# Kernel optimization log

Hardware: AMD Instinct MI355X
Metric: run time of the kernel (lower is better)

The kernel has to match this reference:

```python
import jax, jax.numpy as jnp
import numpy as np

TEMP = 0.1          # temp1 == base_temperature -> scale factor temp/base = 1
N_VIEW = 100        # max_views


def _select_indices(hard, easy):
    """Deterministic analogue of _hard_anchor_sampling's per-(image,class) pick.
    hard, easy: [M, HW] bool. Returns [M, N_VIEW] pixel indices (hard first,
    then easy, in pixel-index order; torch uses randperm but the contrastive
    loss is invariant to which/ordering of in-set samples)."""
    half = N_VIEW // 2
    nh = hard.sum(-1)
    ne = easy.sum(-1)
    both = (nh >= half) & (ne >= half)
    hk = jnp.where(both, half, jnp.where(nh >= half, N_VIEW - ne, nh))  # num_hard_keep
    ek = N_VIEW - hk                                                     # num_easy_keep
    hrank = jnp.cumsum(hard.astype(jnp.int32), -1) - 1
    erank = jnp.cumsum(easy.astype(jnp.int32), -1) - 1
    sel = (hard & (hrank < hk[:, None])) | (easy & (erank < ek[:, None]))
    # stable argsort puts selected pixels first, preserving index order
    order = jnp.argsort(jnp.where(sel, 0, 1), axis=-1)
    return order[:, :N_VIEW]


def _contrastive(feats_, labels_):
    """feats_: [A, V, D], labels_: [A] float. Supervised contrastive loss."""
    A, V, D = feats_.shape
    N = A * V
    # torch.cat(torch.unbind(feats_, 1), 0) -> view-major ordering
    cf = feats_.transpose(1, 0, 2).reshape(N, D)
    lab = jnp.tile(labels_, V)                           # mask.repeat(V, V)
    mask = (lab[:, None] == lab[None, :]).astype(cf.dtype)
    logits = (cf @ cf.T) / TEMP                          # [N, N]
    logits = logits - jax.lax.stop_gradient(logits.max(axis=1, keepdims=True))
    neg_mask = 1.0 - mask                                # before removing diagonal
    pos_mask = mask * (1.0 - jnp.eye(N, dtype=cf.dtype)) # logits_mask zeroes diag
    exp_l = jnp.exp(logits)
    neg_sum = (exp_l * neg_mask).sum(axis=1, keepdims=True)
    log_prob = logits - jnp.log(exp_l + neg_sum)
    mean_log_prob_pos = (pos_mask * log_prob).sum(axis=1) / pos_mask.sum(axis=1)
    return -(TEMP / TEMP) * mean_log_prob_pos.mean()


def _forward(feats, predict, labels):
    B, D, H, W = feats.shape
    C = predict.shape[1]
    HW = H * W
    # F.normalize(feats, p=2, dim=1)
    norm = jnp.sqrt((feats * feats).sum(axis=1, keepdims=True))
    feats = feats / jnp.maximum(norm, 1e-12)
    # bilinear upsample of logits to (H, W), softmax, conf/argmax
    logits_up = jax.image.resize(predict, (B, C, H, W), method='linear')
    probs = jax.nn.softmax(logits_up, axis=1)
    pred = jnp.argmax(probs, axis=1)                     # [B, H, W] (conf unused by loss)
    # nearest resize of labels to (H, W) is identity here (same size)
    pred_f = pred.reshape(B, HW)
    lab_f = labels.reshape(B, HW)
    feats_f = feats.transpose(0, 2, 3, 1).reshape(B, HW, D)
    cls = jnp.arange(C)
    hard = (pred_f[:, None, :] == cls[None, :, None]) & (lab_f[:, None, :] != cls[None, :, None])
    easy = (pred_f[:, None, :] == cls[None, :, None]) & (lab_f[:, None, :] == cls[None, :, None])
    idx = _select_indices(hard.reshape(B * C, HW), easy.reshape(B * C, HW))  # [B*C, N_VIEW]
    b_idx = jnp.repeat(jnp.arange(B), C)
    X_ = feats_f[b_idx[:, None], idx]                    # [B*C, N_VIEW, D]
    y_ = jnp.tile(cls, B).astype(feats.dtype)            # [B*C]
    return _contrastive(X_, y_)


def setup_inputs() -> dict:
    key = jax.random.key(0)
    k1, k2, k3 = jax.random.split(key, 3)
    feats = jax.random.normal(k1, (4, 256, 128, 128), dtype=jnp.float32)
    predict = jax.random.normal(k2, (4, 21, 64, 64), dtype=jnp.float32)
    labels = jax.random.randint(k3, (4, 128, 128), 0, 21, dtype=jnp.int32)
    return {"feats": feats, "predict": predict, "labels": labels}


def reference(feats, predict, labels):
    return _forward(feats, predict, labels)
```

## Files before the change

### kernel.cpp

```cpp
#include <hip/hip_runtime.h>
#include <math.h>

#define HW 16384
#define WID 128
#define BB 4
#define CC 21
#define DD 256
#define NA 84
#define NV 100
#define NN 8400
#define NPOS 400
#define NPAD 8448
#define NTILE 66

typedef __bf16 bf16;
typedef bf16 v8bf __attribute__((ext_vector_type(8)));
typedef float v4f __attribute__((ext_vector_type(4)));

#define AS1(p) ((const __attribute__((address_space(1))) void*)(p))
#define AS3(p) ((__attribute__((address_space(3))) void*)(p))

__global__ void pred_kernel(const float* __restrict__ predict, int* __restrict__ pred) {
  int t = blockIdx.x * blockDim.x + threadIdx.x;
  int b = t / HW;
  int p = t % HW;
  int y = p / WID, x = p % WID;
  float yin = y * 0.5f - 0.25f;
  float xin = x * 0.5f - 0.25f;
  int y0 = (int)floorf(yin), x0 = (int)floorf(xin);
  float fy = yin - (float)y0, fx = xin - (float)x0;
  int y0c = max(y0, 0), y1c = min(y0 + 1, 63);
  int x0c = max(x0, 0), x1c = min(x0 + 1, 63);
  float w00 = (1.f - fy) * (1.f - fx), w01 = (1.f - fy) * fx;
  float w10 = fy * (1.f - fx),        w11 = fy * fx;
  const float* pb = predict + (size_t)b * CC * 4096;
  float best = -1e30f; int bc = 0;
  for (int c = 0; c < CC; ++c) {
    const float* pc = pb + c * 4096;
    float v = w00 * pc[y0c * 64 + x0c] + w01 * pc[y0c * 64 + x1c]
            + w10 * pc[y1c * 64 + x0c] + w11 * pc[y1c * 64 + x1c];
    if (v > best) { best = v; bc = c; }
  }
  pred[t] = bc;
}

__global__ __launch_bounds__(256) void select_kernel(const int* __restrict__ pred,
                                                     const int* __restrict__ labels,
                                                     int* __restrict__ idx) {
  int pair = blockIdx.x;
  int b = pair / CC, c = pair % CC;
  int tid = threadIdx.x;
  const int4* pb = (const int4*)(pred + b * HW) + tid * 16;
  const int4* lb = (const int4*)(labels + b * HW) + tid * 16;

  unsigned long long hm = 0ull, em = 0ull;
  #pragma unroll
  for (int g = 0; g < 16; ++g) {
    int4 p4 = pb[g];
    int4 l4 = lb[g];
    unsigned long long h =
        ((unsigned long long)((p4.x == c) & (l4.x != c)))      |
        ((unsigned long long)((p4.y == c) & (l4.y != c)) << 1) |
        ((unsigned long long)((p4.z == c) & (l4.z != c)) << 2) |
        ((unsigned long long)((p4.w == c) & (l4.w != c)) << 3);
    unsigned long long e =
        ((unsigned long long)((p4.x == c) & (l4.x == c)))      |
        ((unsigned long long)((p4.y == c) & (l4.y == c)) << 1) |
        ((unsigned long long)((p4.z == c) & (l4.z == c)) << 2) |
        ((unsigned long long)((p4.w == c) & (l4.w == c)) << 3);
    hm |= h << (g * 4);
    em |= e << (g * 4);
  }
  int nh_t = __popcll(hm), ne_t = __popcll(em);

  __shared__ int sh[256], se[256], ss[256];
  sh[tid] = nh_t; se[tid] = ne_t;
  __syncthreads();
  for (int off = 1; off < 256; off <<= 1) {
    int vh = (tid >= off) ? sh[tid - off] : 0;
    int ve = (tid >= off) ? se[tid - off] : 0;
    __syncthreads();
    sh[tid] += vh; se[tid] += ve;
    __syncthreads();
  }
  int h_excl = sh[tid] - nh_t, e_excl = se[tid] - ne_t;
  int nh = sh[255], ne = se[255];

  const int half = NV / 2;
  int hk;
  if (nh >= half && ne >= half) hk = half;
  else if (nh >= half)          hk = NV - ne;
  else                          hk = nh;
  int ek = NV - hk;

  int takeh = min(max(hk - h_excl, 0), nh_t);
  int takee = min(max(ek - e_excl, 0), ne_t);
  int sel_t = takeh + takee;
  ss[tid] = sel_t;
  __syncthreads();
  for (int off = 1; off < 256; off <<= 1) {
    int vs = (tid >= off) ? ss[tid - off] : 0;
    __syncthreads();
    ss[tid] += vs;
    __syncthreads();
  }
  int s_excl = ss[tid] - sel_t;
  int total_sel = ss[255];
  int F = NV - total_sel;
  int u_excl = tid * 64 - s_excl;

  int* out = idx + pair * NV;
  int sc = 0, uc = 0, hc = 0, ec = 0;
  for (int l = 0; l < 64; ++l) {
    int p = tid * 64 + l;
    int hard = (int)((hm >> l) & 1ull);
    int easy = (int)((em >> l) & 1ull);
    bool sel = (hard && hc < takeh) || (easy && ec < takee);
    hc += hard; ec += easy;
    if (sel) {
      if (s_excl + sc < NV) out[s_excl + sc] = p;
      sc++;
    } else {
      if (u_excl + uc < F) out[total_sel + u_excl + uc] = p;
      uc++;
    }
  }
}

__global__ __launch_bounds__(256) void gather_kernel(const float* __restrict__ feats,
                                                     const int* __restrict__ idx,
                                                     bf16* __restrict__ cf) {
  int g = blockIdx.x;
  int a = g % NA;
  int v0 = (g / NA) * 4;
  int b = a / CC;
  int d = threadIdx.x;

  int p[4];
  #pragma unroll
  for (int k = 0; k < 4; ++k) p[k] = idx[a * NV + v0 + k];
  const float* base = feats + (size_t)(b * DD + d) * HW;
  float val[4], ssk[4];
  #pragma unroll
  for (int k = 0; k < 4; ++k) { val[k] = base[p[k]]; ssk[k] = val[k] * val[k]; }

  #pragma unroll
  for (int k = 0; k < 4; ++k) {
    float s = ssk[k];
    s += __shfl_xor(s, 1);  s += __shfl_xor(s, 2);  s += __shfl_xor(s, 4);
    s += __shfl_xor(s, 8);  s += __shfl_xor(s, 16); s += __shfl_xor(s, 32);
    ssk[k] = s;
  }
  __shared__ float red[4][4];
  if ((d & 63) == 0) {
    #pragma unroll
    for (int k = 0; k < 4; ++k) red[d >> 6][k] = ssk[k];
  }
  __syncthreads();
  #pragma unroll
  for (int k = 0; k < 4; ++k) {
    float tot = red[0][k] + red[1][k] + red[2][k] + red[3][k];
    float inv = 1.0f / fmaxf(sqrtf(tot), 1e-12f);
    int n = (v0 + k) * NA + a;
    cf[(size_t)n * DD + d] = (bf16)(val[k] * inv);
  }
}

__global__ __launch_bounds__(256) void gemm_kernel(const bf16* __restrict__ cf,
                                                   float* __restrict__ row_part) {
  __shared__ __align__(16) bf16 smem[2 * 128 * 64];
  bf16* sA = smem;
  bf16* sB = smem + 128 * 64;
  int i0 = blockIdx.y * 128;
  int j0 = blockIdx.x * 128;
  int tid = threadIdx.x;
  int wave = tid >> 6, lane = tid & 63;
  int wi = wave >> 1, wj = wave & 1;
  int m = lane & 15, q = lane >> 4;

  v4f acc[4][4] = {};

  int lrow = lane >> 3;
  int lcol = (lane & 7) * 8;

  for (int k0 = 0; k0 < DD; k0 += 64) {
    #pragma unroll
    for (int it = 0; it < 4; ++it) {
      int row = wave * 32 + it * 8;
      const bf16* gA = cf + (size_t)(i0 + row + lrow) * DD + k0 + lcol;
      const bf16* gB = cf + (size_t)(j0 + row + lrow) * DD + k0 + lcol;
      __builtin_amdgcn_global_load_lds(AS1(gA), AS3(sA + row * 64), 16, 0, 0);
      __builtin_amdgcn_global_load_lds(AS1(gB), AS3(sB + row * 64), 16, 0, 0);
    }
    __syncthreads();
    #pragma unroll
    for (int kk = 0; kk < 2; ++kk) {
      v8bf af[4], bfr[4];
      #pragma unroll
      for (int tt = 0; tt < 4; ++tt)
        af[tt] = *(const v8bf*)(sA + (wi * 64 + tt * 16 + m) * 64 + kk * 32 + q * 8);
      #pragma unroll
      for (int tt = 0; tt < 4; ++tt)
        bfr[tt] = *(const v8bf*)(sB + (wj * 64 + tt * 16 + m) * 64 + kk * 32 + q * 8);
      #pragma unroll
      for (int ti = 0; ti < 4; ++ti)
        #pragma unroll
        for (int tj = 0; tj < 4; ++tj)
          acc[ti][tj] = __builtin_amdgcn_mfma_f32_16x16x32_bf16(af[ti], bfr[tj], acc[ti][tj], 0, 0, 0);
    }
    __syncthreads();
  }

  int jw0 = j0 + wj * 64;

  float rowp[16];
  #pragma unroll
  for (int tt = 0; tt < 16; ++tt) rowp[tt] = 0.f;

  #pragma unroll
  for (int ti = 0; ti < 4; ++ti) {
    #pragma unroll
    for (int r = 0; r < 4; ++r) {
      #pragma unroll
      for (int tj = 0; tj < 4; ++tj) {
        int j = jw0 + tj * 16 + m;
        if (j >= NN) continue;
        rowp[ti * 4 + r] += __expf(acc[ti][tj][r] * 10.0f - 10.0f);
      }
    }
  }

  float* red = (float*)smem;
  #pragma unroll
  for (int ti = 0; ti < 4; ++ti)
    #pragma unroll
    for (int r = 0; r < 4; ++r) {
      int rg = wi * 64 + ti * 16 + q * 4 + r;
      red[rg * 33 + wj * 16 + m] = rowp[ti * 4 + r];
    }
  __syncthreads();
  if (tid < 128) {
    float s = 0.f;
    #pragma unroll
    for (int t = 0; t < 32; ++t) s += red[tid * 33 + t];
    row_part[(size_t)blockIdx.x * NPAD + i0 + tid] = s;
  }
}

__global__ __launch_bounds__(256) void pos_gemm_kernel(const bf16* __restrict__ cf,
                                                       float* __restrict__ s_pos) {
  __shared__ __align__(16) bf16 smem[2 * 128 * 64];
  bf16* sA = smem;
  bf16* sB = smem + 128 * 64;
  int c = blockIdx.y;
  int bx = blockIdx.x;
  int i0r = (bx >> 2) * 128;
  int j0r = (bx & 3) * 128;
  int tid = threadIdx.x;
  int wave = tid >> 6, lane = tid & 63;
  int wi = wave >> 1, wj = wave & 1;
  int m = lane & 15, q = lane >> 4;

  v4f acc[4][4] = {};

  int lrow = lane >> 3;
  int lcol = (lane & 7) * 8;

  for (int k0 = 0; k0 < DD; k0 += 64) {
    #pragma unroll
    for (int it = 0; it < 4; ++it) {
      int row = wave * 32 + it * 8;
      int ri = i0r + row + lrow, rj = j0r + row + lrow;
      int gi = (ri < NPOS) ? ((ri >> 2) * NA + (ri & 3) * CC + c) : NN;
      int gj = (rj < NPOS) ? ((rj >> 2) * NA + (rj & 3) * CC + c) : NN;
      const bf16* gA = cf + (size_t)gi * DD + k0 + lcol;
      const bf16* gB = cf + (size_t)gj * DD + k0 + lcol;
      __builtin_amdgcn_global_load_lds(AS1(gA), AS3(sA + row * 64), 16, 0, 0);
      __builtin_amdgcn_global_load_lds(AS1(gB), AS3(sB + row * 64), 16, 0, 0);
    }
    __syncthreads();
    #pragma unroll
    for (int kk = 0; kk < 2; ++kk) {
      v8bf af[4], bfr[4];
      #pragma unroll
      for (int tt = 0; tt < 4; ++tt)
        af[tt] = *(const v8bf*)(sA + (wi * 64 + tt * 16 + m) * 64 + kk * 32 + q * 8);
      #pragma unroll
      for (int tt = 0; tt < 4; ++tt)
        bfr[tt] = *(const v8bf*)(sB + (wj * 64 + tt * 16 + m) * 64 + kk * 32 + q * 8);
      #pragma unroll
      for (int ti = 0; ti < 4; ++ti)
        #pragma unroll
        for (int tj = 0; tj < 4; ++tj)
          acc[ti][tj] = __builtin_amdgcn_mfma_f32_16x16x32_bf16(af[ti], bfr[tj], acc[ti][tj], 0, 0, 0);
    }
    __syncthreads();
  }

  #pragma unroll
  for (int ti = 0; ti < 4; ++ti) {
    #pragma unroll
    for (int r = 0; r < 4; ++r) {
      int ri = i0r + wi * 64 + ti * 16 + q * 4 + r;
      if (ri >= NPOS) continue;
      int gi = (ri >> 2) * NA + (ri & 3) * CC + c;
      #pragma unroll
      for (int tj = 0; tj < 4; ++tj) {
        int rj = j0r + wj * 64 + tj * 16 + m;
        if (rj < NPOS)
          s_pos[(size_t)gi * NPOS + rj] = acc[ti][tj][r] * 10.0f - 10.0f;
      }
    }
  }
}

__global__ __launch_bounds__(256) void loss_kernel(const float* __restrict__ s_pos,
                                                   const float* __restrict__ row_part,
                                                   double* __restrict__ partials) {
  int tid = threadIdx.x;
  int wave = tid >> 6, lane = tid & 63;
  int i = blockIdx.x * 4 + wave;
  const float* row = s_pos + (size_t)i * NPOS;

  float nsum = 0.f;
  for (int jb = lane; jb < NTILE; jb += 64)
    nsum += row_part[(size_t)jb * NPAD + i];

  float sp[7], ev[7];
  float psum = 0.f;
  #pragma unroll
  for (int t = 0; t < 7; ++t) {
    int k = lane + t * 64;
    if (k < NPOS) {
      sp[t] = row[k];
      ev[t] = __expf(sp[t]);
      psum += ev[t];
    } else { sp[t] = 0.f; ev[t] = 0.f; }
  }
  float comb = nsum - psum;
  for (int o = 32; o; o >>= 1) comb += __shfl_xor(comb, o);
  float ns = comb;

  int self = (i / NA) * 4 + ((i % NA) / CC);
  float tsum = 0.f;
  #pragma unroll
  for (int t = 0; t < 7; ++t) {
    int k = lane + t * 64;
    if (k < NPOS && k != self)
      tsum += sp[t] - __logf(ev[t] + ns);
  }
  for (int o = 32; o; o >>= 1) tsum += __shfl_xor(tsum, o);

  __shared__ float r2[4];
  if (lane == 0) r2[wave] = tsum;
  __syncthreads();
  if (tid == 0) partials[blockIdx.x] = (double)(r2[0] + r2[1] + r2[2] + r2[3]);
}

__global__ void final_kernel(const double* __restrict__ partials, float* __restrict__ out) {
  int lane = threadIdx.x;
  double s = 0.0;
  for (int t = lane; t < 2100; t += 64) s += partials[t];
  for (int o = 32; o; o >>= 1) s += __shfl_down(s, o);
  if (lane == 0) out[0] = (float)(-s / 399.0 / 8400.0);
}

extern "C" void kernel_launch(void* const* d_in, const int* in_sizes, int n_in,
                              void* d_out, int out_size, void* d_ws, size_t ws_size,
                              hipStream_t stream) {
  const float* feats   = (const float*)d_in[0];
  const float* predict = (const float*)d_in[1];
  const int*   labels  = (const int*)d_in[2];
  float* out = (float*)d_out;
  char* ws = (char*)d_ws;

  int*    pred     = (int*)(ws + 0);
  int*    idx      = (int*)(ws + 262144);
  float*  row_part = (float*)(ws + 295744);
  double* partials = (double*)(ws + 2526016);
  bf16*   cf       = (bf16*)(ws + 2542816);
  float*  s_pos    = (float*)(ws + 6868192);

  (void)hipMemsetAsync((char*)(cf + (size_t)NN * DD), 0, (size_t)(NPAD - NN) * DD * 2, stream);

  pred_kernel<<<256, 256, 0, stream>>>(predict, pred);
  select_kernel<<<NA, 256, 0, stream>>>(pred, labels, idx);
  gather_kernel<<<2100, 256, 0, stream>>>(feats, idx, cf);
  gemm_kernel<<<dim3(NTILE, NTILE), 256, 0, stream>>>(cf, row_part);
  pos_gemm_kernel<<<dim3(16, CC), 256, 0, stream>>>(cf, s_pos);
  loss_kernel<<<2100, 256, 0, stream>>>(s_pos, row_part, partials);
  final_kernel<<<1, 64, 0, stream>>>(partials, out);
}
```

Measured before the change: 209.7 us.

## Merge positive-pair GEMM into main GEMM launch and XOR-swizzle LDS tiles

Folds the per-class positive-pair GEMM blocks into the main Gram-matrix kernel as extra blocks in a 1D grid, which removes one kernel launch and lets the small pos tiles fill idle CUs in the tail. It also applies an XOR swizzle to the 16-byte column chunks during global->LDS loads and the matching fragment reads, to cut LDS bank conflicts on the MFMA operand loads. The cost is a branch on block type and some extra index arithmetic.

```diff
diff --git a/kernel.cpp b/kernel.cpp
--- a/kernel.cpp
+++ b/kernel.cpp
@@ -12,6 +12,8 @@
 #define NPOS 400
 #define NPAD 8448
 #define NTILE 66
+#define NSQ (NTILE * NTILE)
+#define NPOSBLK (16 * CC)
 
 typedef __bf16 bf16;
 typedef bf16 v8bf __attribute__((ext_vector_type(8)));
@@ -167,12 +169,24 @@
 }
 
 __global__ __launch_bounds__(256) void gemm_kernel(const bf16* __restrict__ cf,
-                                                   float* __restrict__ row_part) {
+                                                   float* __restrict__ row_part,
+                                                   float* __restrict__ s_pos) {
   __shared__ __align__(16) bf16 smem[2 * 128 * 64];
   bf16* sA = smem;
   bf16* sB = smem + 128 * 64;
-  int i0 = blockIdx.y * 128;
-  int j0 = blockIdx.x * 128;
+  int blk = blockIdx.x;
+  bool pos = blk >= NSQ;
+  int i0, j0, c = 0;
+  if (!pos) {
+    i0 = (blk / NTILE) * 128;
+    j0 = (blk % NTILE) * 128;
+  } else {
+    int pb = blk - NSQ;
+    c = pb / 16;
+    int bx = pb % 16;
+    i0 = (bx >> 2) * 128;
+    j0 = (bx & 3) * 128;
+  }
   int tid = threadIdx.x;
   int wave = tid >> 6, lane = tid & 63;
   int wi = wave >> 1, wj = wave & 1;
@@ -181,14 +195,21 @@
   v4f acc[4][4] = {};
 
   int lrow = lane >> 3;
-  int lcol = (lane & 7) * 8;
+  int cxor = (lane & 7) ^ lrow;
 
   for (int k0 = 0; k0 < DD; k0 += 64) {
     #pragma unroll
     for (int it = 0; it < 4; ++it) {
       int row = wave * 32 + it * 8;
-      const bf16* gA = cf + (size_t)(i0 + row + lrow) * DD + k0 + lcol;
-      const bf16* gB = cf + (size_t)(j0 + row + lrow) * DD + k0 + lcol;
+      int ri = i0 + row + lrow, rj = j0 + row + lrow;
+      int gi, gj;
+      if (!pos) { gi = ri; gj = rj; }
+      else {
+        gi = (ri < NPOS) ? ((ri >> 2) * NA + (ri & 3) * CC + c) : NN;
+        gj = (rj < NPOS) ? ((rj >> 2) * NA + (rj & 3) * CC + c) : NN;
+      }
+      const bf16* gA = cf + (size_t)gi * DD + k0 + cxor * 8;
+      const bf16* gB = cf + (size_t)gj * DD + k0 + cxor * 8;
       __builtin_amdgcn_global_load_lds(AS1(gA), AS3(sA + row * 64), 16, 0, 0);
       __builtin_amdgcn_global_load_lds(AS1(gB), AS3(sB + row * 64), 16, 0, 0);
     }
@@ -197,11 +218,15 @@
     for (int kk = 0; kk < 2; ++kk) {
       v8bf af[4], bfr[4];
       #pragma unroll
-      for (int tt = 0; tt < 4; ++tt)
-        af[tt] = *(const v8bf*)(sA + (wi * 64 + tt * 16 + m) * 64 + kk * 32 + q * 8);
-      #pragma unroll
-      for (int tt = 0; tt < 4; ++tt)
-        bfr[tt] = *(const v8bf*)(sB + (wj * 64 + tt * 16 + m) * 64 + kk * 32 + q * 8);
+      for (int tt = 0; tt < 4; ++tt) {
+        int r = wi * 64 + tt * 16 + m;
+        af[tt] = *(const v8bf*)(sA + r * 64 + (((kk * 4 + q) ^ (m & 7)) * 8));
+      }
+      #pragma unroll
+      for (int tt = 0; tt < 4; ++tt) {
+        int r = wj * 64 + tt * 16 + m;
+        bfr[tt] = *(const v8bf*)(sB + r * 64 + (((kk * 4 + q) ^ (m & 7)) * 8));
+      }
       #pragma unroll
       for (int ti = 0; ti < 4; ++ti)
         #pragma unroll
@@ -211,104 +236,54 @@
     __syncthreads();
   }
 
-  int jw0 = j0 + wj * 64;
-
-  float rowp[16];
-  #pragma unroll
-  for (int tt = 0; tt < 16; ++tt) rowp[tt] = 0.f;
-
-  #pragma unroll
-  for (int ti = 0; ti < 4; ++ti) {
-    #pragma unroll
-    for (int r = 0; r < 4; ++r) {
-      #pragma unroll
-      for (int tj = 0; tj < 4; ++tj) {
-        int j = jw0 + tj * 16 + m;
-        if (j >= NN) continue;
-        rowp[ti * 4 + r] += __expf(acc[ti][tj][r] * 10.0f - 10.0f);
-      }
-    }
-  }
-
-  float* red = (float*)smem;
-  #pragma unroll
-  for (int ti = 0; ti < 4; ++ti)
-    #pragma unroll
-    for (int r = 0; r < 4; ++r) {
-      int rg = wi * 64 + ti * 16 + q * 4 + r;
-      red[rg * 33 + wj * 16 + m] = rowp[ti * 4 + r];
-    }
-  __syncthreads();
-  if (tid < 128) {
-    float s = 0.f;
-    #pragma unroll
-    for (int t = 0; t < 32; ++t) s += red[tid * 33 + t];
-    row_part[(size_t)blockIdx.x * NPAD + i0 + tid] = s;
-  }
-}
-
-__global__ __launch_bounds__(256) void pos_gemm_kernel(const bf16* __restrict__ cf,
-                                                       float* __restrict__ s_pos) {
-  __shared__ __align__(16) bf16 smem[2 * 128 * 64];
-  bf16* sA = smem;
-  bf16* sB = smem + 128 * 64;
-  int c = blockIdx.y;
-  int bx = blockIdx.x;
-  int i0r = (bx >> 2) * 128;
-  int j0r = (bx & 3) * 128;
-  int tid = threadIdx.x;
-  int wave = tid >> 6, lane = tid & 63;
-  int wi = wave >> 1, wj = wave & 1;
-  int m = lane & 15, q = lane >> 4;
-
-  v4f acc[4][4] = {};
-
-  int lrow = lane >> 3;
-  int lcol = (lane & 7) * 8;
-
-  for (int k0 = 0; k0 < DD; k0 += 64) {
-    #pragma unroll
-    for (int it = 0; it < 4; ++it) {
-      int row = wave * 32 + it * 8;
-      int ri = i0r + row + lrow, rj = j0r + row + lrow;
-      int gi = (ri < NPOS) ? ((ri >> 2) * NA + (ri & 3) * CC + c) : NN;
-      int gj = (rj < NPOS) ? ((rj >> 2) * NA + (rj & 3) * CC + c) : NN;
-      const bf16* gA = cf + (size_t)gi * DD + k0 + lcol;
-      const bf16* gB = cf + (size_t)gj * DD + k0 + lcol;
-      __builtin_amdgcn_global_load_lds(AS1(gA), AS3(sA + row * 64), 16, 0, 0);
-      __builtin_amdgcn_global_load_lds(AS1(gB), AS3(sB + row * 64), 16, 0, 0);
-    }
-    __syncthreads();
-    #pragma unroll
-    for (int kk = 0; kk < 2; ++kk) {
-      v8bf af[4], bfr[4];
-      #pragma unroll
-      for (int tt = 0; tt < 4; ++tt)
-        af[tt] = *(const v8bf*)(sA + (wi * 64 + tt * 16 + m) * 64 + kk * 32 + q * 8);
-      #pragma unroll
-      for (int tt = 0; tt < 4; ++tt)
-        bfr[tt] = *(const v8bf*)(sB + (wj * 64 + tt * 16 + m) * 64 + kk * 32 + q * 8);
-      #pragma unroll
-      for (int ti = 0; ti < 4; ++ti)
+  if (!pos) {
+    int jw0 = j0 + wj * 64;
+    float rowp[16];
+    #pragma unroll
+    for (int tt = 0; tt < 16; ++tt) rowp[tt] = 0.f;
+
+    #pragma unroll
+    for (int ti = 0; ti < 4; ++ti) {
+      #pragma unroll
+      for (int r = 0; r < 4; ++r) {
         #pragma unroll
-        for (int tj = 0; tj < 4; ++tj)
-          acc[ti][tj] = __builtin_amdgcn_mfma_f32_16x16x32_bf16(af[ti], bfr[tj], acc[ti][tj], 0, 0, 0);
-    }
-    __syncthreads();
-  }
-
-  #pragma unroll
-  for (int ti = 0; ti < 4; ++ti) {
-    #pragma unroll
-    for (int r = 0; r < 4; ++r) {
-      int ri = i0r + wi * 64 + ti * 16 + q * 4 + r;
-      if (ri >= NPOS) continue;
-      int gi = (ri >> 2) * NA + (ri & 3) * CC + c;
-      #pragma unroll
-      for (int tj = 0; tj < 4; ++tj) {
-        int rj = j0r + wj * 64 + tj * 16 + m;
-        if (rj < NPOS)
-          s_pos[(size_t)gi * NPOS + rj] = acc[ti][tj][r] * 10.0f - 10.0f;
+        for (int tj = 0; tj < 4; ++tj) {
+          int j = jw0 + tj * 16 + m;
+          if (j >= NN) continue;
+          rowp[ti * 4 + r] += __expf(acc[ti][tj][r] * 10.0f - 10.0f);
+        }
+      }
+    }
+
+    float* red = (float*)smem;
+    #pragma unroll
+    for (int ti = 0; ti < 4; ++ti)
+      #pragma unroll
+      for (int r = 0; r < 4; ++r) {
+        int rg = wi * 64 + ti * 16 + q * 4 + r;
+        red[rg * 33 + wj * 16 + m] = rowp[ti * 4 + r];
+      }
+    __syncthreads();
+    if (tid < 128) {
+      float s = 0.f;
+      #pragma unroll
+      for (int t = 0; t < 32; ++t) s += red[tid * 33 + t];
+      row_part[(size_t)(blk % NTILE) * NPAD + i0 + tid] = s;
+    }
+  } else {
+    #pragma unroll
+    for (int ti = 0; ti < 4; ++ti) {
+      #pragma unroll
+      for (int r = 0; r < 4; ++r) {
+        int ri = i0 + wi * 64 + ti * 16 + q * 4 + r;
+        if (ri >= NPOS) continue;
+        int gi = (ri >> 2) * NA + (ri & 3) * CC + c;
+        #pragma unroll
+        for (int tj = 0; tj < 4; ++tj) {
+          int rj = j0 + wj * 64 + tj * 16 + m;
+          if (rj < NPOS)
+            s_pos[(size_t)gi * NPOS + rj] = acc[ti][tj][r] * 10.0f - 10.0f;
+        }
       }
     }
   }
@@ -386,8 +361,7 @@
   pred_kernel<<<256, 256, 0, stream>>>(predict, pred);
   select_kernel<<<NA, 256, 0, stream>>>(pred, labels, idx);
   gather_kernel<<<2100, 256, 0, stream>>>(feats, idx, cf);
-  gemm_kernel<<<dim3(NTILE, NTILE), 256, 0, stream>>>(cf, row_part);
-  pos_gemm_kernel<<<dim3(16, CC), 256, 0, stream>>>(cf, s_pos);
+  gemm_kernel<<<NSQ + NPOSBLK, 256, 0, stream>>>(cf, row_part, s_pos);
   loss_kernel<<<2100, 256, 0, stream>>>(s_pos, row_part, partials);
   final_kernel<<<1, 64, 0, stream>>>(partials, out);
 }
```

After: 204.8 us. 1.02x faster.
